# Optimization experiments

Hardware: AMD Instinct MI355X
Metric: run time of the kernel (lower is better)

## Reference

```python
import jax, jax.numpy as jnp
import numpy as np

EPS = 1e-15
PROJ_EPS = 1e-05


def project_hyp_vec(x):
    # clamp squared norm from below at 1 - PROJ_EPS (torch.clamp with min only)
    norm = jnp.sum(x * x, axis=-1, keepdims=True)
    return x * (1.0 - PROJ_EPS) / jnp.maximum(norm, 1.0 - PROJ_EPS)


def atanh(x):
    return 0.5 * jnp.log((1.0 + x) / (1.0 - x))


def mob_add(u, v):
    v = v + EPS
    norm_uv = 2.0 * jnp.sum(u * v, axis=-1, keepdims=True)
    norm_u = jnp.sum(u * u, axis=-1, keepdims=True)
    norm_v = jnp.sum(v * v, axis=-1, keepdims=True)
    denom = 1.0 + norm_uv + norm_v * norm_u
    result = (1.0 + norm_uv + norm_v) / denom * u + (1.0 - norm_u) / denom * v
    return project_hyp_vec(result)


def mob_mat_mul(M, x):
    x = project_hyp_vec(x)
    Mx = x @ M                                   # [B, H]
    Mx_norm = jnp.linalg.norm(Mx + EPS, axis=-1, keepdims=True)
    x_norm = jnp.linalg.norm(x + EPS, axis=-1, keepdims=True)
    return project_hyp_vec(jnp.tanh(Mx_norm / x_norm * atanh(x_norm)) / Mx_norm * Mx)


def setup_inputs() -> dict:
    key = jax.random.key(0)
    k_in, k_w, k_u = jax.random.split(key, 3)
    B, S, I, H = 256, 512, 256, 256
    inputs = jax.random.normal(k_in, (B, S, I), dtype=jnp.float32) * 0.1
    k = (1.0 / H) ** 0.5
    w = jax.random.uniform(k_w, (H, H), minval=-k, maxval=k, dtype=jnp.float32)
    u = jax.random.uniform(k_u, (I, H), minval=-k, maxval=k, dtype=jnp.float32)
    b = jnp.zeros((H,), dtype=jnp.float32)
    return {"inputs": inputs, "w": w, "u": u, "b": b}


def reference(inputs, w, u, b):
    B, S, I = inputs.shape
    H = w.shape[0]

    def step(h, x):
        Wh = mob_mat_mul(w, h)          # [B, H]
        Ux = mob_mat_mul(u, x)          # [B, H]
        h_new = mob_add(mob_add(Wh, Ux), b)
        return h_new, h_new

    h0 = jnp.zeros((B, H), dtype=inputs.dtype)
    _, outs = jax.lax.scan(step, h0, jnp.swapaxes(inputs, 0, 1))  # [S, B, H]
    return jnp.swapaxes(outs, 0, 1)  # [B, S, H]
```

## Files before the change

kernel.cpp:

```cpp
#include <hip/hip_runtime.h>

#define EPSV 1e-15f
#define PEPS 1e-5f

typedef float v2f __attribute__((ext_vector_type(2)));

__device__ __forceinline__ float frcp(float x) { return __builtin_amdgcn_rcpf(x); }
__device__ __forceinline__ float fexp2(float x) { return __builtin_amdgcn_exp2f(x); }
__device__ __forceinline__ float flog2(float x) { return __builtin_amdgcn_logf(x); }
__device__ __forceinline__ float projscale(float n2) {
  return n2 > (1.f - PEPS) ? (1.f - PEPS) * frcp(n2) : 1.f;
}

template <int CTRL>
__device__ __forceinline__ float dppadd(float x) {
  int y = __builtin_amdgcn_update_dpp(0, __float_as_int(x), CTRL, 0xF, 0xF, true);
  return x + __int_as_float(y);
}
__device__ __forceinline__ float wave_sum(float x) {
  x = dppadd<0x111>(x);
  x = dppadd<0x112>(x);
  x = dppadd<0x114>(x);
  x = dppadd<0x118>(x);
  x = dppadd<0x142>(x);
  x = dppadd<0x143>(x);
  return __int_as_float(__builtin_amdgcn_readlane(__float_as_int(x), 63));
}

__global__ __launch_bounds__(256) void ux_kernel(
    const float* __restrict__ x, const float* __restrict__ u,
    const float* __restrict__ bvec, float* __restrict__ out,
    float4* __restrict__ vstat, int use_vstat)
{
  __shared__ __align__(16) float xsT[256][36];

  const int tid = threadIdx.x;
  const int lane = tid & 63, wv = tid >> 6;
  const long long base = (long long)blockIdx.x * 32;

  #pragma unroll
  for (int k4 = 0; k4 < 8; ++k4) {
    float t0 = x[(base + k4 * 4 + 0) * 256 + tid];
    float t1 = x[(base + k4 * 4 + 1) * 256 + tid];
    float t2 = x[(base + k4 * 4 + 2) * 256 + tid];
    float t3 = x[(base + k4 * 4 + 3) * 256 + tid];
    float4 v; v.x = t0; v.y = t1; v.z = t2; v.w = t3;
    *reinterpret_cast<float4*>(&xsT[tid][k4 * 4]) = v;
  }
  __syncthreads();

  float4 bb = *reinterpret_cast<const float4*>(&bvec[4 * lane]);
  bb.x += EPSV; bb.y += EPSV; bb.z += EPSV; bb.w += EPSV;
  float S_vbrow = wave_sum(bb.x + bb.y + bb.z + bb.w);

  float s1[8], s2[8];
  #pragma unroll
  for (int r = 0; r < 8; ++r) { s1[r] = 0.f; s2[r] = 0.f; }
  #pragma unroll
  for (int c = 0; c < 4; ++c) {
    const int i = lane + 64 * c;
    float4 xa = *reinterpret_cast<const float4*>(&xsT[i][8 * wv]);
    float4 xb = *reinterpret_cast<const float4*>(&xsT[i][8 * wv + 4]);
    s1[0] += xa.x; s2[0] += xa.x * xa.x;
    s1[1] += xa.y; s2[1] += xa.y * xa.y;
    s1[2] += xa.z; s2[2] += xa.z * xa.z;
    s1[3] += xa.w; s2[3] += xa.w * xa.w;
    s1[4] += xb.x; s2[4] += xb.x * xb.x;
    s1[5] += xb.y; s2[5] += xb.y * xb.y;
    s1[6] += xb.z; s2[6] += xb.z * xb.z;
    s1[7] += xb.w; s2[7] += xb.w * xb.w;
  }
  float rs[8], xnr[8];
  #pragma unroll
  for (int r = 0; r < 8; ++r) {
    float a = wave_sum(s1[r]);
    float b2 = wave_sum(s2[r]);
    float sc = projscale(b2);
    rs[r] = sc;
    xnr[r] = sqrtf(sc * sc * b2 + 2.f * sc * EPSV * a + 256.f * EPSV * EPSV);
  }

  float4 acc[8];
  #pragma unroll
  for (int r = 0; r < 8; ++r) { acc[r].x = 0.f; acc[r].y = 0.f; acc[r].z = 0.f; acc[r].w = 0.f; }
  #pragma unroll 2
  for (int i = 0; i < 256; ++i) {
    float4 uv = *reinterpret_cast<const float4*>(&u[i * 256 + 4 * lane]);
    float4 xa = *reinterpret_cast<const float4*>(&xsT[i][8 * wv]);
    float4 xb = *reinterpret_cast<const float4*>(&xsT[i][8 * wv + 4]);
    acc[0].x += uv.x * xa.x; acc[0].y += uv.y * xa.x; acc[0].z += uv.z * xa.x; acc[0].w += uv.w * xa.x;
    acc[1].x += uv.x * xa.y; acc[1].y += uv.y * xa.y; acc[1].z += uv.z * xa.y; acc[1].w += uv.w * xa.y;
    acc[2].x += uv.x * xa.z; acc[2].y += uv.y * xa.z; acc[2].z += uv.z * xa.z; acc[2].w += uv.w * xa.z;
    acc[3].x += uv.x * xa.w; acc[3].y += uv.y * xa.w; acc[3].z += uv.z * xa.w; acc[3].w += uv.w * xa.w;
    acc[4].x += uv.x * xb.x; acc[4].y += uv.y * xb.x; acc[4].z += uv.z * xb.x; acc[4].w += uv.w * xb.x;
    acc[5].x += uv.x * xb.y; acc[5].y += uv.y * xb.y; acc[5].z += uv.z * xb.y; acc[5].w += uv.w * xb.y;
    acc[6].x += uv.x * xb.z; acc[6].y += uv.y * xb.z; acc[6].z += uv.z * xb.z; acc[6].w += uv.w * xb.z;
    acc[7].x += uv.x * xb.w; acc[7].y += uv.y * xb.w; acc[7].z += uv.z * xb.w; acc[7].w += uv.w * xb.w;
  }

  #pragma unroll
  for (int r = 0; r < 8; ++r) {
    float t1 = wave_sum(acc[r].x + acc[r].y + acc[r].z + acc[r].w);
    float t2 = wave_sum(acc[r].x * acc[r].x + acc[r].y * acc[r].y +
                        acc[r].z * acc[r].z + acc[r].w * acc[r].w);
    float t3 = wave_sum(acc[r].x * bb.x + acc[r].y * bb.y + acc[r].z * bb.z + acc[r].w * bb.w);
    float Sm  = rs[r] * t1;
    float Sm2 = rs[r] * rs[r] * t2;
    float mxn = sqrtf(Sm2 + 2.f * EPSV * Sm + 256.f * EPSV * EPSV);
    float xn = xnr[r];
    float at = 0.34657359f * flog2((1.f + xn) * frcp(1.f - xn));
    float arg = mxn * frcp(xn) * at;
    float e2 = fexp2(arg * 2.8853902f);
    float th = 1.f - 2.f * frcp(e2 + 1.f);
    float g = th * frcp(mxn);
    float fs = g * projscale(g * g * Sm2) * rs[r];
    float4 o;
    o.x = fs * acc[r].x + EPSV; o.y = fs * acc[r].y + EPSV;
    o.z = fs * acc[r].z + EPSV; o.w = fs * acc[r].w + EPSV;
    reinterpret_cast<float4*>(out)[(base + 8 * wv + r) * 64 + lane] = o;
    if (use_vstat && lane == 0) {
      float Sv  = fs * t1 + 256.f * EPSV;
      float Sv2 = fs * fs * t2 + 2.f * EPSV * fs * t1 + 256.f * EPSV * EPSV;
      float Svb = fs * t3 + EPSV * S_vbrow;
      vstat[base + 8 * wv + r] = float4{Sv, Sv2, Svb, 0.f};
    }
  }
}

template <int NR>
__device__ __forceinline__ void load_w(const float* __restrict__ w, int rb, int lane, v2f* wr) {
  #pragma unroll
  for (int r = 0; r < NR; ++r) {
    float4 t = *reinterpret_cast<const float4*>(&w[(rb + r) * 256 + 4 * lane]);
    asm volatile("" : "+v"(t.x), "+v"(t.y), "+v"(t.z), "+v"(t.w));
    wr[2 * r]     = v2f{t.x, t.y};
    wr[2 * r + 1] = v2f{t.z, t.w};
  }
}

#define NLDSROW 112

template <int NREG>
__device__ __forceinline__ void mv_step(const float (*Wl)[256], const v2f* wr,
                                        int ldsb, int regb, int lane,
                                        const float* mxp, const float* vp,
                                        float* pPrw, float* pQrw) {
  v2f pl{0.f,0.f}, ph{0.f,0.f}, ql{0.f,0.f}, qh{0.f,0.f};
  #pragma unroll
  for (int i = 0; i < 2; ++i) {
    float4 h4 = *reinterpret_cast<const float4*>(mxp + ldsb + 4 * i);
    float4 u4 = *reinterpret_cast<const float4*>(vp + ldsb + 4 * i);
    float hh[4] = {h4.x, h4.y, h4.z, h4.w};
    float uu[4] = {u4.x, u4.y, u4.z, u4.w};
    #pragma unroll
    for (int j = 0; j < 4; ++j) {
      float4 w4 = *reinterpret_cast<const float4*>(&Wl[ldsb + 4 * i + j][4 * lane]);
      v2f wl{w4.x, w4.y}, wh{w4.z, w4.w};
      pl += wl * hh[j]; ph += wh * hh[j];
      ql += wl * uu[j]; qh += wh * uu[j];
    }
  }
  #pragma unroll
  for (int i = 0; i < NREG / 4; ++i) {
    float4 h4 = *reinterpret_cast<const float4*>(mxp + regb + 4 * i);
    float4 u4 = *reinterpret_cast<const float4*>(vp + regb + 4 * i);
    float hh[4] = {h4.x, h4.y, h4.z, h4.w};
    float uu[4] = {u4.x, u4.y, u4.z, u4.w};
    #pragma unroll
    for (int j = 0; j < 4; ++j) {
      v2f wl = wr[8 * i + 2 * j], wh = wr[8 * i + 2 * j + 1];
      pl += wl * hh[j]; ph += wh * hh[j];
      ql += wl * uu[j]; qh += wh * uu[j];
    }
  }
  *reinterpret_cast<float4*>(pPrw + 4 * lane) = float4{pl.x, pl.y, ph.x, ph.y};
  *reinterpret_cast<float4*>(pQrw + 4 * lane) = float4{ql.x, ql.y, qh.x, qh.y};
}

__global__ __launch_bounds__(1024) void rnn_kernel(
    const float* __restrict__ w, const float* __restrict__ bvec,
    float* __restrict__ out, const float4* __restrict__ vstat, int S, int use_vstat)
{
  __shared__ __align__(16) float W_lds[NLDSROW][256];
  __shared__ __align__(16) float mx_lds[256];
  __shared__ __align__(16) float v_lds[2][256];
  __shared__ __align__(16) float wvb_lds[256];
  __shared__ __align__(16) float pP[16][256];
  __shared__ __align__(16) float pQ[16][256];
  __shared__ float sc_lds[4];

  const int tid = threadIdx.x;
  const int lane = tid & 63;
  const int wv = tid >> 6;

  const long long rb4 = (long long)blockIdx.x * S * 64;
  const long long vsbase = (long long)blockIdx.x * S;
  const float4* outv = reinterpret_cast<const float4*>(out);
  float4* outw = reinterpret_cast<float4*>(out);
  const float4 zero4{0.f, 0.f, 0.f, 0.f};

  {
    const float4* w4 = reinterpret_cast<const float4*>(w);
    float4* wl4 = reinterpret_cast<float4*>(&W_lds[0][0]);
    #pragma unroll
    for (int c = 0; c < 7; ++c) {
      int idx = c * 1024 + tid;
      wl4[idx] = w4[idx];
    }
  }

  if (wv == 0) {
    float4 vb4 = *reinterpret_cast<const float4*>(&bvec[4 * lane]);
    vb4.x += EPSV; vb4.y += EPSV; vb4.z += EPSV; vb4.w += EPSV;
    float S_vb  = wave_sum(vb4.x + vb4.y + vb4.z + vb4.w);
    float S_vb2 = wave_sum(vb4.x * vb4.x + vb4.y * vb4.y + vb4.z * vb4.z + vb4.w * vb4.w);

    reinterpret_cast<float4*>(mx_lds)[lane] = zero4;
    reinterpret_cast<float4*>(v_lds[0])[lane] = vb4;
    __syncthreads();
    __syncthreads();

    float sAx = 0.f, sAy = 0.f, sAz = 0.f;
    if (use_vstat) { float4 s = vstat[vsbase]; sAx = s.x; sAy = s.y; sAz = s.z; }
    __syncthreads();

    float S_h = 0.f, S_h2 = 0.f;

    for (int t = 0; t < S; ++t) {
      const int b = t & 1;
      float4 m4 = *reinterpret_cast<const float4*>(&mx_lds[4 * lane]);
      float4 v4 = *reinterpret_cast<const float4*>(&v_lds[b][4 * lane]);

      float nsx = 0.f, nsy = 0.f, nsz = 0.f;
      if (use_vstat && t + 1 < S) { float4 s = vstat[vsbase + t + 1]; nsx = s.x; nsy = s.y; nsz = s.z; }

      float S_Mx  = wave_sum(m4.x + m4.y + m4.z + m4.w);
      float S_Mx2 = wave_sum(m4.x * m4.x + m4.y * m4.y + m4.z * m4.z + m4.w * m4.w);
      float S_Mxv = wave_sum(m4.x * v4.x + m4.y * v4.y + m4.z * v4.z + m4.w * v4.w);
      float S_Mxb = wave_sum(m4.x * vb4.x + m4.y * vb4.y + m4.z * vb4.z + m4.w * vb4.w);
      float S_v, S_v2, S_vvb;
      if (use_vstat) { S_v = sAx; S_v2 = sAy; S_vvb = sAz; }
      else {
        S_v   = wave_sum(v4.x + v4.y + v4.z + v4.w);
        S_v2  = wave_sum(v4.x * v4.x + v4.y * v4.y + v4.z * v4.z + v4.w * v4.w);
        S_vvb = wave_sum(v4.x * vb4.x + v4.y * vb4.y + v4.z * vb4.z + v4.w * vb4.w);
      }

      float s_hp = projscale(S_h2);
      float xn = sqrtf(s_hp * s_hp * S_h2 + 2.f * s_hp * EPSV * S_h + 256.f * EPSV * EPSV);
      float mxn = sqrtf(S_Mx2 + 2.f * EPSV * S_Mx + 256.f * EPSV * EPSV);
      float at = 0.34657359f * flog2((1.f + xn) * frcp(1.f - xn));
      float arg = mxn * frcp(xn) * at;
      float e2 = fexp2(arg * 2.8853902f);
      float th = 1.f - 2.f * frcp(e2 + 1.f);
      float g = th * frcp(mxn);
      float beta = g * projscale(g * g * S_Mx2);

      float nuv = 2.f * beta * S_Mxv;
      float nu  = beta * beta * S_Mx2;
      float nv  = S_v2;
      float rden = frcp(1.f + nuv + nv * nu);
      float cA = (1.f + nuv + nv) * rden;
      float cB = (1.f - nu) * rden;
      float cAb = cA * beta;
      float S_r1  = cAb * S_Mx + cB * S_v;
      float S_r12 = cAb * cAb * S_Mx2 + 2.f * cAb * cB * S_Mxv + cB * cB * S_v2;
      float S_r1b = cAb * S_Mxb + cB * S_vvb;
      float s1p = projscale(S_r12);
      float S_U = s1p * S_r1, S_U2 = s1p * s1p * S_r12, S_Ub = s1p * S_r1b;

      float nuv2 = 2.f * S_Ub;
      float rden2 = frcp(1.f + nuv2 + S_vb2 * S_U2);
      float dA = (1.f + nuv2 + S_vb2) * rden2;
      float dB = (1.f - S_U2) * rden2;
      float S_hn  = dA * S_U + dB * S_vb;
      float S_hn2 = dA * dA * S_U2 + 2.f * dA * dB * S_Ub + dB * dB * S_vb2;
      float s2p = projscale(S_hn2);

      float km = s2p * dA * s1p * cAb;
      float kv = s2p * dA * s1p * cB;
      float kb = s2p * dB;

      float4 hn{km * m4.x + kv * v4.x + kb * vb4.x,
                km * m4.y + kv * v4.y + kb * vb4.y,
                km * m4.z + kv * v4.z + kb * vb4.z,
                km * m4.w + kv * v4.w + kb * vb4.w};
      outw[rb4 + (long long)t * 64 + lane] = hn;

      S_h  = s2p * S_hn;
      S_h2 = s2p * s2p * S_hn2;
      float snextp = projscale(S_h2);

      if (lane == 0) {
        sc_lds[0] = snextp * km;
        sc_lds[1] = snextp * kv;
        sc_lds[2] = snextp * kb;
      }

      __syncthreads();
      __syncthreads();

      sAx = nsx; sAy = nsy; sAz = nsz;
    }
  } else if (wv == 1) {
    float4 vA = outv[rb4 + lane];
    float4 vB = outv[rb4 + 64 + lane];
    float4 vC = outv[rb4 + 128 + lane];
    __syncthreads();
    __syncthreads();
    {
      const int c = lane;
      float qc = 0.f;
      #pragma unroll
      for (int k = 2; k < 16; ++k) qc += pQ[k][c];
      wvb_lds[c] = qc;
      reinterpret_cast<float4*>(v_lds[0])[lane] = vA;
    }
    __syncthreads();

    for (int t = 0; t < S; ++t) {
      if (t + 1 < S) reinterpret_cast<float4*>(v_lds[(t + 1) & 1])[lane] = vB;
      vB = vC;
      if (t + 3 < S) vC = outv[rb4 + (long long)(t + 3) * 64 + lane];
      __syncthreads();
      {
        const int c = lane;
        float s0 = sc_lds[0], s1 = sc_lds[1], s2 = sc_lds[2];
        float pc = 0.f, qc = 0.f;
        #pragma unroll
        for (int k = 2; k < 16; ++k) { pc += pP[k][c]; qc += pQ[k][c]; }
        mx_lds[c] = s0 * pc + s1 * qc + s2 * wvb_lds[c];
      }
      __syncthreads();
    }
  } else if (wv <= 9) {
    const int ldsb = 8 * (wv - 2);
    const int regb = 112 + 12 * (wv - 2);
    v2f wr[24];
    load_w<12>(w, regb, lane, wr);
    __syncthreads();
    mv_step<12>(W_lds, wr, ldsb, regb, lane, mx_lds, v_lds[0], pP[wv], pQ[wv]);
    __syncthreads();
    __syncthreads();
    for (int t = 0; t < S; ++t) {
      const int b = t & 1;
      mv_step<12>(W_lds, wr, ldsb, regb, lane, mx_lds, v_lds[b], pP[wv], pQ[wv]);
      __syncthreads();
      __syncthreads();
    }
  } else {
    const int ldsb = 8 * (wv - 2);
    const int regb = 208 + 8 * (wv - 10);
    const bool docmb = (wv >= 13);
    const int c = 64 * (wv - 12) + lane;
    v2f wr[16];
    load_w<8>(w, regb, lane, wr);
    __syncthreads();
    mv_step<8>(W_lds, wr, ldsb, regb, lane, mx_lds, v_lds[0], pP[wv], pQ[wv]);
    __syncthreads();
    if (docmb) {
      float qc = 0.f;
      #pragma unroll
      for (int k = 2; k < 16; ++k) qc += pQ[k][c];
      wvb_lds[c] = qc;
    }
    __syncthreads();
    for (int t = 0; t < S; ++t) {
      const int b = t & 1;
      mv_step<8>(W_lds, wr, ldsb, regb, lane, mx_lds, v_lds[b], pP[wv], pQ[wv]);
      __syncthreads();
      if (docmb) {
        float s0 = sc_lds[0], s1 = sc_lds[1], s2 = sc_lds[2];
        float pc = 0.f, qc = 0.f;
        #pragma unroll
        for (int k = 2; k < 16; ++k) { pc += pP[k][c]; qc += pQ[k][c]; }
        mx_lds[c] = s0 * pc + s1 * qc + s2 * wvb_lds[c];
      }
      __syncthreads();
    }
  }
}

extern "C" void kernel_launch(void* const* d_in, const int* in_sizes, int n_in,
                              void* d_out, int out_size, void* d_ws, size_t ws_size,
                              hipStream_t stream) {
  const float* x = (const float*)d_in[0];
  const float* w = (const float*)d_in[1];
  const float* u = (const float*)d_in[2];
  const float* b = (const float*)d_in[3];
  float* out = (float*)d_out;

  const int nrows = in_sizes[0] / 256;
  const int S = 512;
  const int B = nrows / S;

  const int use_vstat = (ws_size >= (size_t)nrows * 16) ? 1 : 0;
  float4* vstat = (float4*)d_ws;

  ux_kernel<<<nrows / 32, 256, 0, stream>>>(x, u, b, out, vstat, use_vstat);
  rnn_kernel<<<B, 1024, 0, stream>>>(w, b, out, vstat, S, use_vstat);
}
```

Before: 911.7 us.

## Store recurrent weight in LDS as fp16 and shrink block to nine waves

Converts the full 256x256 recurrent weight matrix to half precision so it fits entirely in LDS, replacing the split between LDS rows and register-held rows. The workgroup shrinks from 16 waves to 9: 8 waves each handle 32 rows of the matrix-vector product (including the previously dedicated helper wave), and there are fewer partial-sum rows to reduce. This cuts register pressure, the partial-reduction work and barrier participants per step. In exchange, every step pays half-to-float conversion, and the fp16 weights lose precision, which may accumulate error over 512 recurrent steps.

```diff
diff --git a/kernel.cpp b/kernel.cpp
--- a/kernel.cpp
+++ b/kernel.cpp
@@ -1,4 +1,5 @@
 #include <hip/hip_runtime.h>
+#include <hip/hip_fp16.h>
 
 #define EPSV 1e-15f
 #define PEPS 1e-5f
@@ -127,66 +128,42 @@
   }
 }
 
-template <int NR>
-__device__ __forceinline__ void load_w(const float* __restrict__ w, int rb, int lane, v2f* wr) {
-  #pragma unroll
-  for (int r = 0; r < NR; ++r) {
-    float4 t = *reinterpret_cast<const float4*>(&w[(rb + r) * 256 + 4 * lane]);
-    asm volatile("" : "+v"(t.x), "+v"(t.y), "+v"(t.z), "+v"(t.w));
-    wr[2 * r]     = v2f{t.x, t.y};
-    wr[2 * r + 1] = v2f{t.z, t.w};
-  }
-}
-
-#define NLDSROW 112
-
-template <int NREG>
-__device__ __forceinline__ void mv_step(const float (*Wl)[256], const v2f* wr,
-                                        int ldsb, int regb, int lane,
-                                        const float* mxp, const float* vp,
-                                        float* pPrw, float* pQrw) {
-  v2f pl{0.f,0.f}, ph{0.f,0.f}, ql{0.f,0.f}, qh{0.f,0.f};
-  #pragma unroll
-  for (int i = 0; i < 2; ++i) {
-    float4 h4 = *reinterpret_cast<const float4*>(mxp + ldsb + 4 * i);
-    float4 u4 = *reinterpret_cast<const float4*>(vp + ldsb + 4 * i);
-    float hh[4] = {h4.x, h4.y, h4.z, h4.w};
-    float uu[4] = {u4.x, u4.y, u4.z, u4.w};
+__device__ __forceinline__ void mv16(const __half* __restrict__ Wl, int rbase, int lane,
+                                     const float* __restrict__ mxp,
+                                     const float* __restrict__ vp,
+                                     float* __restrict__ Pout, float* __restrict__ Qout) {
+  v2f p0{0.f,0.f}, p1{0.f,0.f}, q0{0.f,0.f}, q1{0.f,0.f};
+  #pragma unroll
+  for (int g = 0; g < 8; ++g) {
+    float4 m4 = *reinterpret_cast<const float4*>(mxp + rbase + 4 * g);
+    float4 v4 = *reinterpret_cast<const float4*>(vp + rbase + 4 * g);
+    float mm[4] = {m4.x, m4.y, m4.z, m4.w};
+    float vv[4] = {v4.x, v4.y, v4.z, v4.w};
     #pragma unroll
-    for (int j = 0; j < 4; ++j) {
-      float4 w4 = *reinterpret_cast<const float4*>(&Wl[ldsb + 4 * i + j][4 * lane]);
-      v2f wl{w4.x, w4.y}, wh{w4.z, w4.w};
-      pl += wl * hh[j]; ph += wh * hh[j];
-      ql += wl * uu[j]; qh += wh * uu[j];
-    }
-  }
-  #pragma unroll
-  for (int i = 0; i < NREG / 4; ++i) {
-    float4 h4 = *reinterpret_cast<const float4*>(mxp + regb + 4 * i);
-    float4 u4 = *reinterpret_cast<const float4*>(vp + regb + 4 * i);
-    float hh[4] = {h4.x, h4.y, h4.z, h4.w};
-    float uu[4] = {u4.x, u4.y, u4.z, u4.w};
-    #pragma unroll
-    for (int j = 0; j < 4; ++j) {
-      v2f wl = wr[8 * i + 2 * j], wh = wr[8 * i + 2 * j + 1];
-      pl += wl * hh[j]; ph += wh * hh[j];
-      ql += wl * uu[j]; qh += wh * uu[j];
-    }
-  }
-  *reinterpret_cast<float4*>(pPrw + 4 * lane) = float4{pl.x, pl.y, ph.x, ph.y};
-  *reinterpret_cast<float4*>(pQrw + 4 * lane) = float4{ql.x, ql.y, qh.x, qh.y};
-}
-
-__global__ __launch_bounds__(1024) void rnn_kernel(
+    for (int r = 0; r < 4; ++r) {
+      const int i = rbase + 4 * g + r;
+      const __half2* wp = reinterpret_cast<const __half2*>(Wl + (size_t)i * 256 + 4 * lane);
+      float2 wa = __half22float2(wp[0]);
+      float2 wb = __half22float2(wp[1]);
+      v2f wa2{wa.x, wa.y}, wb2{wb.x, wb.y};
+      p0 += wa2 * mm[r]; p1 += wb2 * mm[r];
+      q0 += wa2 * vv[r]; q1 += wb2 * vv[r];
+    }
+  }
+  *reinterpret_cast<float4*>(Pout + 4 * lane) = float4{p0.x, p0.y, p1.x, p1.y};
+  *reinterpret_cast<float4*>(Qout + 4 * lane) = float4{q0.x, q0.y, q1.x, q1.y};
+}
+
+__global__ __launch_bounds__(576) void rnn_kernel(
     const float* __restrict__ w, const float* __restrict__ bvec,
     float* __restrict__ out, const float4* __restrict__ vstat, int S, int use_vstat)
 {
-  __shared__ __align__(16) float W_lds[NLDSROW][256];
+  __shared__ __align__(16) __half w16[256][256];
   __shared__ __align__(16) float mx_lds[256];
   __shared__ __align__(16) float v_lds[2][256];
   __shared__ __align__(16) float wvb_lds[256];
-  __shared__ __align__(16) float pP[16][256];
-  __shared__ __align__(16) float pQ[16][256];
+  __shared__ __align__(16) float pP[8][256];
+  __shared__ __align__(16) float pQ[8][256];
   __shared__ float sc_lds[4];
 
   const int tid = threadIdx.x;
@@ -201,11 +178,11 @@
 
   {
     const float4* w4 = reinterpret_cast<const float4*>(w);
-    float4* wl4 = reinterpret_cast<float4*>(&W_lds[0][0]);
-    #pragma unroll
-    for (int c = 0; c < 7; ++c) {
-      int idx = c * 1024 + tid;
-      wl4[idx] = w4[idx];
+    __half2* W2 = reinterpret_cast<__half2*>(&w16[0][0]);
+    for (int idx = tid; idx < 16384; idx += 576) {
+      float4 t = w4[idx];
+      W2[2 * idx]     = __floats2half2_rn(t.x, t.y);
+      W2[2 * idx + 1] = __floats2half2_rn(t.z, t.w);
     }
   }
 
@@ -303,22 +280,26 @@
       sAx = nsx; sAy = nsy; sAz = nsz;
     }
   } else if (wv == 1) {
+    const int rbase = 0;
     float4 vA = outv[rb4 + lane];
     float4 vB = outv[rb4 + 64 + lane];
     float4 vC = outv[rb4 + 128 + lane];
     __syncthreads();
+    mv16(&w16[0][0], rbase, lane, mx_lds, v_lds[0], pP[0], pQ[0]);
     __syncthreads();
     {
       const int c = lane;
       float qc = 0.f;
       #pragma unroll
-      for (int k = 2; k < 16; ++k) qc += pQ[k][c];
+      for (int k = 0; k < 8; ++k) qc += pQ[k][c];
       wvb_lds[c] = qc;
       reinterpret_cast<float4*>(v_lds[0])[lane] = vA;
     }
     __syncthreads();
 
     for (int t = 0; t < S; ++t) {
+      const int b = t & 1;
+      mv16(&w16[0][0], rbase, lane, mx_lds, v_lds[b], pP[0], pQ[0]);
       if (t + 1 < S) reinterpret_cast<float4*>(v_lds[(t + 1) & 1])[lane] = vB;
       vB = vC;
       if (t + 3 < S) vC = outv[rb4 + (long long)(t + 3) * 64 + lane];
@@ -328,54 +309,47 @@
         float s0 = sc_lds[0], s1 = sc_lds[1], s2 = sc_lds[2];
         float pc = 0.f, qc = 0.f;
         #pragma unroll
-        for (int k = 2; k < 16; ++k) { pc += pP[k][c]; qc += pQ[k][c]; }
+        for (int k = 0; k < 8; ++k) { pc += pP[k][c]; qc += pQ[k][c]; }
         mx_lds[c] = s0 * pc + s1 * qc + s2 * wvb_lds[c];
       }
       __syncthreads();
     }
-  } else if (wv <= 9) {
-    const int ldsb = 8 * (wv - 2);
-    const int regb = 112 + 12 * (wv - 2);
-    v2f wr[24];
-    load_w<12>(w, regb, lane, wr);
-    __syncthreads();
-    mv_step<12>(W_lds, wr, ldsb, regb, lane, mx_lds, v_lds[0], pP[wv], pQ[wv]);
-    __syncthreads();
+  } else if (wv <= 4) {
+    const int rbase = 32 * (wv - 1);
+    const int c = 64 * (wv - 1) + lane;
+    __syncthreads();
+    mv16(&w16[0][0], rbase, lane, mx_lds, v_lds[0], pP[wv - 1], pQ[wv - 1]);
+    __syncthreads();
+    {
+      float qc = 0.f;
+      #pragma unroll
+      for (int k = 0; k < 8; ++k) qc += pQ[k][c];
+      wvb_lds[c] = qc;
+    }
     __syncthreads();
     for (int t = 0; t < S; ++t) {
       const int b = t & 1;
-      mv_step<12>(W_lds, wr, ldsb, regb, lane, mx_lds, v_lds[b], pP[wv], pQ[wv]);
-      __syncthreads();
-      __syncthreads();
-    }
-  } else {
-    const int ldsb = 8 * (wv - 2);
-    const int regb = 208 + 8 * (wv - 10);
-    const bool docmb = (wv >= 13);
-    const int c = 64 * (wv - 12) + lane;
-    v2f wr[16];
-    load_w<8>(w, regb, lane, wr);
-    __syncthreads();
-    mv_step<8>(W_lds, wr, ldsb, regb, lane, mx_lds, v_lds[0], pP[wv], pQ[wv]);
-    __syncthreads();
-    if (docmb) {
-      float qc = 0.f;
-      #pragma unroll
-      for (int k = 2; k < 16; ++k) qc += pQ[k][c];
-      wvb_lds[c] = qc;
-    }
-    __syncthreads();
-    for (int t = 0; t < S; ++t) {
-      const int b = t & 1;
-      mv_step<8>(W_lds, wr, ldsb, regb, lane, mx_lds, v_lds[b], pP[wv], pQ[wv]);
-      __syncthreads();
-      if (docmb) {
+      mv16(&w16[0][0], rbase, lane, mx_lds, v_lds[b], pP[wv - 1], pQ[wv - 1]);
+      __syncthreads();
+      {
         float s0 = sc_lds[0], s1 = sc_lds[1], s2 = sc_lds[2];
         float pc = 0.f, qc = 0.f;
         #pragma unroll
-        for (int k = 2; k < 16; ++k) { pc += pP[k][c]; qc += pQ[k][c]; }
+        for (int k = 0; k < 8; ++k) { pc += pP[k][c]; qc += pQ[k][c]; }
         mx_lds[c] = s0 * pc + s1 * qc + s2 * wvb_lds[c];
       }
+      __syncthreads();
+    }
+  } else {
+    const int rbase = 32 * (wv - 1);
+    __syncthreads();
+    mv16(&w16[0][0], rbase, lane, mx_lds, v_lds[0], pP[wv - 1], pQ[wv - 1]);
+    __syncthreads();
+    __syncthreads();
+    for (int t = 0; t < S; ++t) {
+      const int b = t & 1;
+      mv16(&w16[0][0], rbase, lane, mx_lds, v_lds[b], pP[wv - 1], pQ[wv - 1]);
+      __syncthreads();
       __syncthreads();
     }
   }
@@ -398,5 +372,5 @@
   float4* vstat = (float4*)d_ws;
 
   ux_kernel<<<nrows / 32, 256, 0, stream>>>(x, u, b, out, vstat, use_vstat);
-  rnn_kernel<<<B, 1024, 0, stream>>>(w, b, out, vstat, S, use_vstat);
-}
+  rnn_kernel<<<B, 576, 0, stream>>>(w, b, out, vstat, S, use_vstat);
+}
```

Measured after the change: 1.151 ms. +26.2%, slower.
